# Performance work log

Hardware: AMD Instinct MI355X
Metric: run time of the kernel (lower is better)

Reference implementation:

```python
import jax, jax.numpy as jnp
import numpy as np

N_NODES = 100000
N_EDGES = 1200000
IN_CH = 64
HID = 64


def sage_conv(x, src, dst, Wl, b, Wr, num_nodes):
    # mean aggregation of source-node features at target nodes (flow=source_to_target)
    msg = x[src]                                      # [E, C] gather
    agg = jax.ops.segment_sum(msg, dst, num_segments=num_nodes)  # [N, C]
    cnt = jax.ops.segment_sum(jnp.ones((src.shape[0],), x.dtype), dst,
                              num_segments=num_nodes)
    mean = agg / jnp.maximum(cnt, 1.0)[:, None]
    # PyG SAGEConv: lin_l(aggregated) + bias + lin_r(root)
    return mean @ Wl + b + x @ Wr


def setup_inputs() -> dict:
    key = jax.random.key(0)
    ks = jax.random.split(key, 10)
    x = jax.random.normal(ks[0], (N_NODES, IN_CH), dtype=jnp.float32)
    edge_index = jax.random.randint(ks[1], (2, N_EDGES), 0, N_NODES, dtype=jnp.int64)
    s1 = 1.0 / np.sqrt(IN_CH)
    s2 = 1.0 / np.sqrt(HID)
    W1l = jax.random.uniform(ks[2], (IN_CH, HID), jnp.float32, -s1, s1)
    b1 = jax.random.uniform(ks[3], (HID,), jnp.float32, -s1, s1)
    W1r = jax.random.uniform(ks[4], (IN_CH, HID), jnp.float32, -s1, s1)
    W2l = jax.random.uniform(ks[5], (HID, HID), jnp.float32, -s2, s2)
    b2 = jax.random.uniform(ks[6], (HID,), jnp.float32, -s2, s2)
    W2r = jax.random.uniform(ks[7], (HID, HID), jnp.float32, -s2, s2)
    Wfc = jax.random.uniform(ks[8], (HID, 1), jnp.float32, -s2, s2)
    bfc = jax.random.uniform(ks[9], (1,), jnp.float32, -s2, s2)
    return {"x": x, "edge_index": edge_index, "W1l": W1l, "b1": b1, "W1r": W1r,
            "W2l": W2l, "b2": b2, "W2r": W2r, "Wfc": Wfc, "bfc": bfc}


def reference(x, edge_index, W1l, b1, W1r, W2l, b2, W2r, Wfc, bfc):
    num_nodes = x.shape[0]
    src, dst = edge_index[0], edge_index[1]
    x = jnp.nan_to_num(x, nan=0.0)
    # layer 1: SAGEConv -> ReLU (dropout is identity in eval)
    h = jax.nn.relu(sage_conv(x, src, dst, W1l, b1, W1r, num_nodes))
    # layer 2
    h = jax.nn.relu(sage_conv(h, src, dst, W2l, b2, W2r, num_nodes))
    pred = (h @ Wfc + bfc)[:, 0]  # (num_nodes,)
    return pred
```

## Files before the change

kernel.cpp:

```cpp
#include <hip/hip_runtime.h>

#define NN_NODES 100000
#define NN_EDGES 1200000
#define CH 64
#define BUCKET_NODES 200
#define NBUCKETS (NN_NODES / BUCKET_NODES)
#define EPB 4096
#define PASSA_THREADS 1024
#define XCDS 8
#define PCAP 768
#define BMAX (XCDS * PCAP)

typedef __attribute__((ext_vector_type(8))) short bf16x8;
typedef __attribute__((ext_vector_type(4))) float f32x4;

__device__ __forceinline__ float nan0(float v) { return v == v ? v : 0.0f; }

__device__ __forceinline__ unsigned short f2bf(float f) {
    unsigned u = __float_as_uint(f);
    return (unsigned short)((u + 0x7fffu + ((u >> 16) & 1u)) >> 16);
}

__device__ __forceinline__ unsigned xcc_id() {
    unsigned x;
    asm volatile("s_getreg_b32 %0, hwreg(HW_REG_XCC_ID)" : "=s"(x));
    return x & (XCDS - 1);
}

__global__ __launch_bounds__(256) void convert_kernel(
    const float* __restrict__ x, unsigned short* __restrict__ xb, int n4)
{
    int i = blockIdx.x * 256 + threadIdx.x;
    if (i >= n4) return;
    float4 v = ((const float4*)x)[i];
    v.x = nan0(v.x); v.y = nan0(v.y); v.z = nan0(v.z); v.w = nan0(v.w);
    ushort4 o;
    o.x = f2bf(v.x); o.y = f2bf(v.y); o.z = f2bf(v.z); o.w = f2bf(v.w);
    ((ushort4*)xb)[i] = o;
}

__global__ __launch_bounds__(256) void wprep_kernel(
    const float* __restrict__ W1l, const float* __restrict__ W1r,
    const float* __restrict__ W2l, const float* __restrict__ W2r,
    unsigned short* __restrict__ Wt1, unsigned short* __restrict__ Wt2)
{
    int i = blockIdx.x * 256 + threadIdx.x;
    if (i >= 64 * 128) return;
    int n = i >> 7;
    int k = i & 127;
    float v1 = (k < 64) ? W1l[k * 64 + n] : W1r[(k - 64) * 64 + n];
    float v2 = (k < 64) ? W2l[k * 64 + n] : W2r[(k - 64) * 64 + n];
    Wt1[i] = f2bf(v1);
    Wt2[i] = f2bf(v2);
}

__global__ __launch_bounds__(PASSA_THREADS) void passA_kernel(
    const int* __restrict__ src, const int* __restrict__ dst,
    int* __restrict__ bcnt, unsigned int* __restrict__ bbuf, int nEdges)
{
    __shared__ int lhist[NBUCKETS];
    __shared__ int lbase[NBUCKETS];
    int tid = threadIdx.x;
    int e0 = blockIdx.x * EPB;
    unsigned xcc = xcc_id();

    for (int i = tid; i < NBUCKETS; i += PASSA_THREADS) lhist[i] = 0;
    __syncthreads();

    int eb = e0 + tid * 4;
    int nv = nEdges - eb;
    if (nv > 4) nv = 4;
    int da[4] = {-1, -1, -1, -1};
    if (nv == 4) {
        int4 dv = *(const int4*)(dst + eb);
        da[0] = dv.x; da[1] = dv.y; da[2] = dv.z; da[3] = dv.w;
    } else {
        for (int r = 0; r < nv; r++) da[r] = dst[eb + r];
    }
    #pragma unroll
    for (int r = 0; r < 4; r++)
        if (da[r] >= 0) atomicAdd(&lhist[da[r] / BUCKET_NODES], 1);
    __syncthreads();

    for (int i = tid; i < NBUCKETS; i += PASSA_THREADS) {
        int c = lhist[i];
        lbase[i] = c > 0 ? atomicAdd(&bcnt[i * XCDS + xcc], c) : 0;
        lhist[i] = 0;
    }
    __syncthreads();

    int sa[4] = {0, 0, 0, 0};
    if (nv == 4) {
        int4 sv = *(const int4*)(src + eb);
        sa[0] = sv.x; sa[1] = sv.y; sa[2] = sv.z; sa[3] = sv.w;
    } else {
        for (int r = 0; r < nv; r++) sa[r] = src[eb + r];
    }
    #pragma unroll
    for (int r = 0; r < 4; r++) {
        int d = da[r];
        if (d >= 0) {
            int b = d / BUCKET_NODES;
            int dloc = d - b * BUCKET_NODES;
            int pos = lbase[b] + atomicAdd(&lhist[b], 1);
            if (pos < PCAP)
                bbuf[((size_t)b * XCDS + xcc) * PCAP + pos] =
                    ((unsigned)dloc << 24) | (unsigned)sa[r];
        }
    }
}

__global__ __launch_bounds__(512) void scan_bcnt_kernel(
    const int* __restrict__ bcnt, int* __restrict__ bbase,
    int* __restrict__ rowptr)
{
    __shared__ int s[512];
    int t = threadIdx.x;
    int own = 0;
    if (t < NBUCKETS) {
        #pragma unroll
        for (int x = 0; x < XCDS; x++) {
            int c = bcnt[t * XCDS + x];
            own += c < PCAP ? c : PCAP;
        }
    }
    s[t] = own;
    __syncthreads();
    for (int off = 1; off < 512; off <<= 1) {
        int v = (t >= off) ? s[t - off] : 0;
        __syncthreads();
        s[t] += v;
        __syncthreads();
    }
    if (t < NBUCKETS) bbase[t] = s[t] - own;
    if (t == NBUCKETS - 1) rowptr[NN_NODES] = s[t];
}

__global__ __launch_bounds__(256) void passB_kernel(
    const int* __restrict__ bcnt, const int* __restrict__ bbase,
    const unsigned int* __restrict__ bbuf,
    int* __restrict__ col, int* __restrict__ rowptr)
{
    __shared__ int hist[BUCKET_NODES];
    __shared__ int cur[BUCKET_NODES];
    __shared__ int sc[256];
    __shared__ unsigned int stage[BMAX];
    int b = blockIdx.x;
    int t = threadIdx.x;
    int base = bbase[b];

    for (int i = t; i < BUCKET_NODES; i += 256) hist[i] = 0;
    __syncthreads();

    int cnt = 0;
    #pragma unroll
    for (int x = 0; x < XCDS; x++) {
        int pc = bcnt[b * XCDS + x];
        if (pc > PCAP) pc = PCAP;
        const unsigned int* seg = bbuf + ((size_t)b * XCDS + x) * PCAP;
        for (int k = t; k < pc; k += 256) {
            unsigned v = seg[k];
            stage[cnt + k] = v;
            atomicAdd(&hist[v >> 24], 1);
        }
        cnt += pc;
    }
    __syncthreads();

    int own = (t < BUCKET_NODES) ? hist[t] : 0;
    sc[t] = own;
    __syncthreads();
    for (int off = 1; off < 256; off <<= 1) {
        int v = (t >= off) ? sc[t - off] : 0;
        __syncthreads();
        sc[t] += v;
        __syncthreads();
    }
    if (t < BUCKET_NODES) {
        int excl = sc[t] - own;
        rowptr[b * BUCKET_NODES + t] = base + excl;
        cur[t] = excl;
    }
    __syncthreads();

    for (int k = t; k < cnt; k += 256) {
        unsigned v = stage[k];
        int dloc = (int)(v >> 24);
        int pos = atomicAdd(&cur[dloc], 1);
        col[base + pos] = (int)(v & 0xFFFFFFu);
    }
}

__global__ __launch_bounds__(256) void gather_kernel(
    const unsigned short* __restrict__ xb,
    const int* __restrict__ rowptr, const int* __restrict__ col,
    unsigned short* __restrict__ mgb, int nNodes)
{
    int w    = threadIdx.x >> 6;
    int lane = threadIdx.x & 63;
    int sub  = lane >> 4;
    int l16  = lane & 15;
    int node = blockIdx.x * 4 + w;
    if (node >= nNodes) return;
    int r0 = rowptr[node], r1 = rowptr[node + 1];
    float a0[4] = {0, 0, 0, 0}, a1[4] = {0, 0, 0, 0};
    int i = r0 + sub;
    for (; i + 4 < r1; i += 8) {
        int s0 = col[i];
        int s1 = col[i + 4];
        uint2 u0 = *(const uint2*)(xb + (size_t)s0 * CH + l16 * 4);
        uint2 u1 = *(const uint2*)(xb + (size_t)s1 * CH + l16 * 4);
        a0[0] += __uint_as_float(u0.x << 16);
        a0[1] += __uint_as_float(u0.x & 0xffff0000u);
        a0[2] += __uint_as_float(u0.y << 16);
        a0[3] += __uint_as_float(u0.y & 0xffff0000u);
        a1[0] += __uint_as_float(u1.x << 16);
        a1[1] += __uint_as_float(u1.x & 0xffff0000u);
        a1[2] += __uint_as_float(u1.y << 16);
        a1[3] += __uint_as_float(u1.y & 0xffff0000u);
    }
    if (i < r1) {
        int s0 = col[i];
        uint2 u0 = *(const uint2*)(xb + (size_t)s0 * CH + l16 * 4);
        a0[0] += __uint_as_float(u0.x << 16);
        a0[1] += __uint_as_float(u0.x & 0xffff0000u);
        a0[2] += __uint_as_float(u0.y << 16);
        a0[3] += __uint_as_float(u0.y & 0xffff0000u);
    }
    #pragma unroll
    for (int j = 0; j < 4; j++) a0[j] += a1[j];
    #pragma unroll
    for (int j = 0; j < 4; j++) {
        a0[j] += __shfl_xor(a0[j], 16, 64);
        a0[j] += __shfl_xor(a0[j], 32, 64);
    }
    if (lane < 16) {
        int deg = r1 - r0;
        float inv = 1.0f / (float)(deg > 0 ? deg : 1);
        ushort4 o;
        o.x = f2bf(a0[0] * inv); o.y = f2bf(a0[1] * inv);
        o.z = f2bf(a0[2] * inv); o.w = f2bf(a0[3] * inv);
        *(ushort4*)(mgb + (size_t)node * CH + l16 * 4) = o;
    }
}

template<int LAYER>
__global__ __launch_bounds__(256) void dense_kernel(
    const unsigned short* __restrict__ rootb,
    const unsigned short* __restrict__ mgb,
    const unsigned short* __restrict__ Wt,
    const float* __restrict__ bias,
    const float* __restrict__ Wfc, const float* __restrict__ bfc,
    unsigned short* __restrict__ hb_out,
    float* __restrict__ out,
    int nNodes)
{
    __shared__ unsigned short sA[64][136];
    __shared__ unsigned short sW[64][136];
    __shared__ unsigned short sO[64][72];

    int tid = threadIdx.x;
    int n_base = blockIdx.x * 64;

    {
        const uint4* g = (const uint4*)Wt;
        for (int i = tid; i < 1024; i += 256) {
            int n = i >> 4;
            int c = i & 15;
            *(uint4*)&sW[n][c * 8] = g[i];
        }
    }
    {
        for (int i = tid; i < 1024; i += 256) {
            int node = i >> 4;
            int c = i & 15;
            int gn = n_base + node;
            if (gn >= nNodes) gn = nNodes - 1;
            const unsigned short* srcp = (c < 8)
                ? (mgb + (size_t)gn * CH + c * 8)
                : (rootb + (size_t)gn * CH + (c - 8) * 8);
            *(uint4*)&sA[node][c * 8] = *(const uint4*)srcp;
        }
    }
    __syncthreads();

    int wave = tid >> 6;
    int lane = tid & 63;
    int quad = lane >> 4;
    int colx = lane & 15;
    int m0 = wave * 16;

    f32x4 acc[4];
    #pragma unroll
    for (int nt = 0; nt < 4; nt++) acc[nt] = (f32x4){0.f, 0.f, 0.f, 0.f};

    #pragma unroll
    for (int ks = 0; ks < 4; ks++) {
        bf16x8 af = *(const bf16x8*)&sA[m0 + colx][ks * 32 + quad * 8];
        #pragma unroll
        for (int nt = 0; nt < 4; nt++) {
            bf16x8 bfr = *(const bf16x8*)&sW[nt * 16 + colx][ks * 32 + quad * 8];
            acc[nt] = __builtin_amdgcn_mfma_f32_16x16x32_bf16(af, bfr, acc[nt], 0, 0, 0);
        }
    }

    float bv[4];
    #pragma unroll
    for (int nt = 0; nt < 4; nt++) bv[nt] = bias[nt * 16 + colx];

    if (LAYER == 1) {
        #pragma unroll
        for (int nt = 0; nt < 4; nt++)
            #pragma unroll
            for (int r = 0; r < 4; r++) {
                float v = acc[nt][r] + bv[nt];
                v = v > 0.f ? v : 0.f;
                sO[m0 + quad * 4 + r][nt * 16 + colx] = f2bf(v);
            }
        __syncthreads();
        for (int i = tid; i < 512; i += 256) {
            int node = i >> 3;
            int c = i & 7;
            int gn = n_base + node;
            if (gn < nNodes)
                *(uint4*)(hb_out + (size_t)gn * CH + c * 8) =
                    *(const uint4*)&sO[node][c * 8];
        }
    } else {
        float wf[4];
        #pragma unroll
        for (int nt = 0; nt < 4; nt++) wf[nt] = Wfc[nt * 16 + colx];
        float bfc0 = bfc[0];
        #pragma unroll
        for (int r = 0; r < 4; r++) {
            float p = 0.f;
            #pragma unroll
            for (int nt = 0; nt < 4; nt++) {
                float v = acc[nt][r] + bv[nt];
                v = v > 0.f ? v : 0.f;
                p += v * wf[nt];
            }
            p += __shfl_xor(p, 1, 64);
            p += __shfl_xor(p, 2, 64);
            p += __shfl_xor(p, 4, 64);
            p += __shfl_xor(p, 8, 64);
            if (colx == 0) {
                int gn = n_base + m0 + quad * 4 + r;
                if (gn < nNodes) out[gn] = p + bfc0;
            }
        }
    }
}

extern "C" void kernel_launch(void* const* d_in, const int* in_sizes, int n_in,
                              void* d_out, int out_size, void* d_ws, size_t ws_size,
                              hipStream_t stream) {
    const float* x    = (const float*)d_in[0];
    const int*   ei   = (const int*)d_in[1];
    const float* W1l  = (const float*)d_in[2];
    const float* b1   = (const float*)d_in[3];
    const float* W1r  = (const float*)d_in[4];
    const float* W2l  = (const float*)d_in[5];
    const float* b2   = (const float*)d_in[6];
    const float* W2r  = (const float*)d_in[7];
    const float* Wfc  = (const float*)d_in[8];
    const float* bfc  = (const float*)d_in[9];
    float* out = (float*)d_out;

    const int N = NN_NODES;
    const int E = NN_EDGES;
    const int* src = ei;
    const int* dst = ei + E;

    char* ws = (char*)d_ws;
    unsigned short* xb  = (unsigned short*)ws;  ws += (size_t)N * CH * sizeof(unsigned short);
    unsigned short* h1b = (unsigned short*)ws;  ws += (size_t)N * CH * sizeof(unsigned short);
    unsigned short* mgb = (unsigned short*)ws;  ws += (size_t)N * CH * sizeof(unsigned short);
    unsigned short* Wt1 = (unsigned short*)ws;  ws += 64 * 128 * sizeof(unsigned short);
    unsigned short* Wt2 = (unsigned short*)ws;  ws += 64 * 128 * sizeof(unsigned short);
    int* bcnt   = (int*)ws;                     ws += (size_t)NBUCKETS * XCDS * sizeof(int);
    int* bbase  = (int*)ws;                     ws += 512 * sizeof(int);
    int* rowptr = (int*)ws;                     ws += (size_t)(N + 1) * sizeof(int);
    int* col    = (int*)ws;                     ws += (size_t)E * sizeof(int);
    unsigned int* bbuf = (unsigned int*)mgb;

    hipMemsetAsync(bcnt, 0, (size_t)NBUCKETS * XCDS * sizeof(int), stream);

    convert_kernel<<<(N * CH / 4 + 255) / 256, 256, 0, stream>>>(x, xb, N * CH / 4);
    wprep_kernel<<<32, 256, 0, stream>>>(W1l, W1r, W2l, W2r, Wt1, Wt2);
    passA_kernel<<<(E + EPB - 1) / EPB, PASSA_THREADS, 0, stream>>>(
        src, dst, bcnt, bbuf, E);
    scan_bcnt_kernel<<<1, 512, 0, stream>>>(bcnt, bbase, rowptr);
    passB_kernel<<<NBUCKETS, 256, 0, stream>>>(bcnt, bbase, bbuf, col, rowptr);

    int gblocks = (N + 3) / 4;
    int dblocks = (N + 63) / 64;

    gather_kernel<<<gblocks, 256, 0, stream>>>(xb, rowptr, col, mgb, N);
    dense_kernel<1><<<dblocks, 256, 0, stream>>>(
        xb, mgb, Wt1, b1, nullptr, nullptr, h1b, nullptr, N);
    gather_kernel<<<gblocks, 256, 0, stream>>>(h1b, rowptr, col, mgb, N);
    dense_kernel<2><<<dblocks, 256, 0, stream>>>(
        h1b, mgb, Wt2, b2, Wfc, bfc, nullptr, out, N);
}
```

Measured before the change: 224.0 us.

## Fuse prep kernels into one launch and fold bucket scan into passB

Merges the feature conversion, weight transpose and edge-bucketing pass into a single kernel whose blocks branch on block index. It also removes the single-block scan kernel: each passB block now sums the clamped bucket counts of all earlier buckets itself to find its base offset. This drops three kernel launches and their serialization gaps. In exchange, each passB block redundantly reads up to 4000 counts, and the merged kernel runs the convert and weight work with 1024-thread blocks that carry the bucketing pass's shared-memory footprint.

```diff
diff --git a/kernel.cpp b/kernel.cpp
--- a/kernel.cpp
+++ b/kernel.cpp
@@ -6,10 +6,16 @@
 #define BUCKET_NODES 200
 #define NBUCKETS (NN_NODES / BUCKET_NODES)
 #define EPB 4096
-#define PASSA_THREADS 1024
+#define PREP_THREADS 1024
 #define XCDS 8
 #define PCAP 768
 #define BMAX (XCDS * PCAP)
+
+#define PA_BLOCKS ((NN_EDGES + EPB - 1) / EPB)
+#define CV_ITEMS (NN_NODES * CH / 4)
+#define CV_BLOCKS ((CV_ITEMS + PREP_THREADS - 1) / PREP_THREADS)
+#define WP_ITEMS (64 * 128)
+#define WP_BLOCKS ((WP_ITEMS + PREP_THREADS - 1) / PREP_THREADS)
 
 typedef __attribute__((ext_vector_type(8))) short bf16x8;
 typedef __attribute__((ext_vector_type(4))) float f32x4;
@@ -27,118 +33,91 @@
     return x & (XCDS - 1);
 }
 
-__global__ __launch_bounds__(256) void convert_kernel(
-    const float* __restrict__ x, unsigned short* __restrict__ xb, int n4)
-{
-    int i = blockIdx.x * 256 + threadIdx.x;
-    if (i >= n4) return;
-    float4 v = ((const float4*)x)[i];
-    v.x = nan0(v.x); v.y = nan0(v.y); v.z = nan0(v.z); v.w = nan0(v.w);
-    ushort4 o;
-    o.x = f2bf(v.x); o.y = f2bf(v.y); o.z = f2bf(v.z); o.w = f2bf(v.w);
-    ((ushort4*)xb)[i] = o;
-}
-
-__global__ __launch_bounds__(256) void wprep_kernel(
+__global__ __launch_bounds__(PREP_THREADS) void prep_kernel(
+    const float* __restrict__ x, unsigned short* __restrict__ xb,
     const float* __restrict__ W1l, const float* __restrict__ W1r,
     const float* __restrict__ W2l, const float* __restrict__ W2r,
-    unsigned short* __restrict__ Wt1, unsigned short* __restrict__ Wt2)
-{
-    int i = blockIdx.x * 256 + threadIdx.x;
-    if (i >= 64 * 128) return;
-    int n = i >> 7;
-    int k = i & 127;
-    float v1 = (k < 64) ? W1l[k * 64 + n] : W1r[(k - 64) * 64 + n];
-    float v2 = (k < 64) ? W2l[k * 64 + n] : W2r[(k - 64) * 64 + n];
-    Wt1[i] = f2bf(v1);
-    Wt2[i] = f2bf(v2);
-}
-
-__global__ __launch_bounds__(PASSA_THREADS) void passA_kernel(
+    unsigned short* __restrict__ Wt1, unsigned short* __restrict__ Wt2,
     const int* __restrict__ src, const int* __restrict__ dst,
-    int* __restrict__ bcnt, unsigned int* __restrict__ bbuf, int nEdges)
+    int* __restrict__ bcnt, unsigned int* __restrict__ bbuf)
 {
     __shared__ int lhist[NBUCKETS];
     __shared__ int lbase[NBUCKETS];
     int tid = threadIdx.x;
-    int e0 = blockIdx.x * EPB;
-    unsigned xcc = xcc_id();
-
-    for (int i = tid; i < NBUCKETS; i += PASSA_THREADS) lhist[i] = 0;
-    __syncthreads();
-
-    int eb = e0 + tid * 4;
-    int nv = nEdges - eb;
-    if (nv > 4) nv = 4;
-    int da[4] = {-1, -1, -1, -1};
-    if (nv == 4) {
-        int4 dv = *(const int4*)(dst + eb);
-        da[0] = dv.x; da[1] = dv.y; da[2] = dv.z; da[3] = dv.w;
+    int bid = blockIdx.x;
+
+    if (bid < PA_BLOCKS) {
+        int e0 = bid * EPB;
+        unsigned xcc = xcc_id();
+
+        for (int i = tid; i < NBUCKETS; i += PREP_THREADS) lhist[i] = 0;
+        __syncthreads();
+
+        int eb = e0 + tid * 4;
+        int nv = NN_EDGES - eb;
+        if (nv > 4) nv = 4;
+        int da[4] = {-1, -1, -1, -1};
+        if (nv == 4) {
+            int4 dv = *(const int4*)(dst + eb);
+            da[0] = dv.x; da[1] = dv.y; da[2] = dv.z; da[3] = dv.w;
+        } else {
+            for (int r = 0; r < nv; r++) da[r] = dst[eb + r];
+        }
+        #pragma unroll
+        for (int r = 0; r < 4; r++)
+            if (da[r] >= 0) atomicAdd(&lhist[da[r] / BUCKET_NODES], 1);
+        __syncthreads();
+
+        for (int i = tid; i < NBUCKETS; i += PREP_THREADS) {
+            int c = lhist[i];
+            lbase[i] = c > 0 ? atomicAdd(&bcnt[i * XCDS + xcc], c) : 0;
+            lhist[i] = 0;
+        }
+        __syncthreads();
+
+        int sa[4] = {0, 0, 0, 0};
+        if (nv == 4) {
+            int4 sv = *(const int4*)(src + eb);
+            sa[0] = sv.x; sa[1] = sv.y; sa[2] = sv.z; sa[3] = sv.w;
+        } else {
+            for (int r = 0; r < nv; r++) sa[r] = src[eb + r];
+        }
+        #pragma unroll
+        for (int r = 0; r < 4; r++) {
+            int d = da[r];
+            if (d >= 0) {
+                int b = d / BUCKET_NODES;
+                int dloc = d - b * BUCKET_NODES;
+                int pos = lbase[b] + atomicAdd(&lhist[b], 1);
+                if (pos < PCAP)
+                    bbuf[((size_t)b * XCDS + xcc) * PCAP + pos] =
+                        ((unsigned)dloc << 24) | (unsigned)sa[r];
+            }
+        }
+    } else if (bid < PA_BLOCKS + CV_BLOCKS) {
+        int i = (bid - PA_BLOCKS) * PREP_THREADS + tid;
+        if (i < CV_ITEMS) {
+            float4 v = ((const float4*)x)[i];
+            v.x = nan0(v.x); v.y = nan0(v.y); v.z = nan0(v.z); v.w = nan0(v.w);
+            ushort4 o;
+            o.x = f2bf(v.x); o.y = f2bf(v.y); o.z = f2bf(v.z); o.w = f2bf(v.w);
+            ((ushort4*)xb)[i] = o;
+        }
     } else {
-        for (int r = 0; r < nv; r++) da[r] = dst[eb + r];
-    }
-    #pragma unroll
-    for (int r = 0; r < 4; r++)
-        if (da[r] >= 0) atomicAdd(&lhist[da[r] / BUCKET_NODES], 1);
-    __syncthreads();
-
-    for (int i = tid; i < NBUCKETS; i += PASSA_THREADS) {
-        int c = lhist[i];
-        lbase[i] = c > 0 ? atomicAdd(&bcnt[i * XCDS + xcc], c) : 0;
-        lhist[i] = 0;
-    }
-    __syncthreads();
-
-    int sa[4] = {0, 0, 0, 0};
-    if (nv == 4) {
-        int4 sv = *(const int4*)(src + eb);
-        sa[0] = sv.x; sa[1] = sv.y; sa[2] = sv.z; sa[3] = sv.w;
-    } else {
-        for (int r = 0; r < nv; r++) sa[r] = src[eb + r];
-    }
-    #pragma unroll
-    for (int r = 0; r < 4; r++) {
-        int d = da[r];
-        if (d >= 0) {
-            int b = d / BUCKET_NODES;
-            int dloc = d - b * BUCKET_NODES;
-            int pos = lbase[b] + atomicAdd(&lhist[b], 1);
-            if (pos < PCAP)
-                bbuf[((size_t)b * XCDS + xcc) * PCAP + pos] =
-                    ((unsigned)dloc << 24) | (unsigned)sa[r];
-        }
-    }
-}
-
-__global__ __launch_bounds__(512) void scan_bcnt_kernel(
-    const int* __restrict__ bcnt, int* __restrict__ bbase,
-    int* __restrict__ rowptr)
-{
-    __shared__ int s[512];
-    int t = threadIdx.x;
-    int own = 0;
-    if (t < NBUCKETS) {
-        #pragma unroll
-        for (int x = 0; x < XCDS; x++) {
-            int c = bcnt[t * XCDS + x];
-            own += c < PCAP ? c : PCAP;
-        }
-    }
-    s[t] = own;
-    __syncthreads();
-    for (int off = 1; off < 512; off <<= 1) {
-        int v = (t >= off) ? s[t - off] : 0;
-        __syncthreads();
-        s[t] += v;
-        __syncthreads();
-    }
-    if (t < NBUCKETS) bbase[t] = s[t] - own;
-    if (t == NBUCKETS - 1) rowptr[NN_NODES] = s[t];
+        int i = (bid - PA_BLOCKS - CV_BLOCKS) * PREP_THREADS + tid;
+        if (i < WP_ITEMS) {
+            int n = i >> 7;
+            int k = i & 127;
+            float v1 = (k < 64) ? W1l[k * 64 + n] : W1r[(k - 64) * 64 + n];
+            float v2 = (k < 64) ? W2l[k * 64 + n] : W2r[(k - 64) * 64 + n];
+            Wt1[i] = f2bf(v1);
+            Wt2[i] = f2bf(v2);
+        }
+    }
 }
 
 __global__ __launch_bounds__(256) void passB_kernel(
-    const int* __restrict__ bcnt, const int* __restrict__ bbase,
-    const unsigned int* __restrict__ bbuf,
+    const int* __restrict__ bcnt, const unsigned int* __restrict__ bbuf,
     int* __restrict__ col, int* __restrict__ rowptr)
 {
     __shared__ int hist[BUCKET_NODES];
@@ -147,9 +126,23 @@
     __shared__ unsigned int stage[BMAX];
     int b = blockIdx.x;
     int t = threadIdx.x;
-    int base = bbase[b];
 
     for (int i = t; i < BUCKET_NODES; i += 256) hist[i] = 0;
+
+    int part = 0;
+    int lim = b * XCDS;
+    for (int i = t; i < lim; i += 256) {
+        int c = bcnt[i];
+        part += c > PCAP ? PCAP : c;
+    }
+    sc[t] = part;
+    __syncthreads();
+    #pragma unroll
+    for (int off = 128; off > 0; off >>= 1) {
+        if (t < off) sc[t] += sc[t + off];
+        __syncthreads();
+    }
+    int base = sc[0];
     __syncthreads();
 
     int cnt = 0;
@@ -181,6 +174,7 @@
         rowptr[b * BUCKET_NODES + t] = base + excl;
         cur[t] = excl;
     }
+    if (b == NBUCKETS - 1 && t == 0) rowptr[NN_NODES] = base + cnt;
     __syncthreads();
 
     for (int k = t; k < cnt; k += 256) {
@@ -379,19 +373,15 @@
     unsigned short* Wt1 = (unsigned short*)ws;  ws += 64 * 128 * sizeof(unsigned short);
     unsigned short* Wt2 = (unsigned short*)ws;  ws += 64 * 128 * sizeof(unsigned short);
     int* bcnt   = (int*)ws;                     ws += (size_t)NBUCKETS * XCDS * sizeof(int);
-    int* bbase  = (int*)ws;                     ws += 512 * sizeof(int);
     int* rowptr = (int*)ws;                     ws += (size_t)(N + 1) * sizeof(int);
     int* col    = (int*)ws;                     ws += (size_t)E * sizeof(int);
     unsigned int* bbuf = (unsigned int*)mgb;
 
     hipMemsetAsync(bcnt, 0, (size_t)NBUCKETS * XCDS * sizeof(int), stream);
 
-    convert_kernel<<<(N * CH / 4 + 255) / 256, 256, 0, stream>>>(x, xb, N * CH / 4);
-    wprep_kernel<<<32, 256, 0, stream>>>(W1l, W1r, W2l, W2r, Wt1, Wt2);
-    passA_kernel<<<(E + EPB - 1) / EPB, PASSA_THREADS, 0, stream>>>(
-        src, dst, bcnt, bbuf, E);
-    scan_bcnt_kernel<<<1, 512, 0, stream>>>(bcnt, bbase, rowptr);
-    passB_kernel<<<NBUCKETS, 256, 0, stream>>>(bcnt, bbase, bbuf, col, rowptr);
+    prep_kernel<<<PA_BLOCKS + CV_BLOCKS + WP_BLOCKS, PREP_THREADS, 0, stream>>>(
+        x, xb, W1l, W1r, W2l, W2r, Wt1, Wt2, src, dst, bcnt, bbuf);
+    passB_kernel<<<NBUCKETS, 256, 0, stream>>>(bcnt, bbuf, col, rowptr);
 
     int gblocks = (N + 3) / 4;
     int dblocks = (N + 63) / 64;
```

Result: faster. 214.5 us (-4.3%).
